# Kernel tuning notes

Measured on AMD Instinct MI355X. Metric: run time of the kernel, lower is better.

## Reference

```python
import jax, jax.numpy as jnp
import numpy as np

D_MODEL = 1024
NUM_HEADS = 16
D_FF = 4096
EPS = 1e-5


def setup_inputs() -> dict:
    key = jax.random.key(0)
    ks = jax.random.split(key, 8)
    B, S, D = 4, 2048, D_MODEL
    s = 1.0 / np.sqrt(D)
    return {
        "x": jax.random.normal(ks[0], (B, S, D), jnp.float32),
        "ln1_w": jnp.ones((D,), jnp.float32),
        "ln2_w": jnp.ones((D,), jnp.float32),
        "wq": jax.random.normal(ks[1], (D, D), jnp.float32) * s,
        "wk": jax.random.normal(ks[2], (D, D), jnp.float32) * s,
        "wv": jax.random.normal(ks[3], (D, D), jnp.float32) * s,
        "wo": jax.random.normal(ks[4], (D, D), jnp.float32) * s,
        "w1": jax.random.normal(ks[5], (D_FF, D), jnp.float32) * s,
        "w2": jax.random.normal(ks[6], (D, D_FF), jnp.float32) * (1.0 / np.sqrt(D_FF)),
    }


def rmsnorm(a, w):
    # (a * w) / sqrt(mean(a^2) + eps)  -- matches torch module exactly
    denom = jnp.sqrt(jnp.mean(jnp.square(a), axis=-1, keepdims=True) + EPS)
    return a * w / denom


def attention(x, wq, wk, wv, wo):
    B, S, D = x.shape
    H, dk = NUM_HEADS, D // NUM_HEADS
    q = (x @ wq.T).reshape(B, S, H, dk).transpose(0, 2, 1, 3)  # B H S dk
    k = (x @ wk.T).reshape(B, S, H, dk).transpose(0, 2, 1, 3)
    v = (x @ wv.T).reshape(B, S, H, dk).transpose(0, 2, 1, 3)
    scores = jnp.einsum("bhqd,bhkd->bhqk", q, k) / np.sqrt(dk)
    causal = jnp.triu(jnp.ones((S, S), bool), k=1)
    scores = jnp.where(causal, -jnp.inf, scores)
    probs = jax.nn.softmax(scores, axis=-1)
    out = jnp.einsum("bhqk,bhkd->bhqd", probs, v)
    out = out.transpose(0, 2, 1, 3).reshape(B, S, D)
    return out @ wo.T


def ffn(x, w1, w2):
    h = x @ w1.T
    h = 0.5 * h * (1.0 + jax.lax.erf(h / np.sqrt(2.0).astype(np.float32)))
    return h @ w2.T


def reference(x, ln1_w, ln2_w, wq, wk, wv, wo, w1, w2):
    y = x + attention(rmsnorm(x, ln1_w), wq, wk, wv, wo)
    return y + ffn(rmsnorm(y, ln2_w), w1, w2)
```

## Files before the change

kernel.cpp:

```cpp
#include <hip/hip_runtime.h>

#define DM    1024
#define DFF   4096
#define SEQ   2048
#define BATCH 4
#define NROWS (BATCH * SEQ)
#define HEADS 16
#define DKH   64
#define QSTR  (3 * DM)

typedef __attribute__((ext_vector_type(4))) float          f32x4;
typedef __attribute__((ext_vector_type(8))) __bf16         bf16x8;
typedef __attribute__((ext_vector_type(8))) unsigned short u16x8;
typedef __attribute__((ext_vector_type(4))) unsigned short u16x4;

static __device__ __forceinline__ unsigned short f2bf(float f) {
  unsigned u = __builtin_bit_cast(unsigned, f);
  u += 0x7fffu + ((u >> 16) & 1u);
  return (unsigned short)(u >> 16);
}

__global__ void k_f2bf(const float* __restrict__ in, unsigned short* __restrict__ out, int n4) {
  int i = blockIdx.x * blockDim.x + threadIdx.x;
  if (i >= n4) return;
  float4 v = reinterpret_cast<const float4*>(in)[i];
  ushort4 o;
  o.x = f2bf(v.x); o.y = f2bf(v.y); o.z = f2bf(v.z); o.w = f2bf(v.w);
  reinterpret_cast<ushort4*>(out)[i] = o;
}

__global__ __launch_bounds__(256) void k_rmsnorm(const float* __restrict__ x,
                                                 const float* __restrict__ w,
                                                 unsigned short* __restrict__ out) {
  const int row = blockIdx.x;
  const float4 v = reinterpret_cast<const float4*>(x + (size_t)row * DM)[threadIdx.x];
  float ss = v.x * v.x + v.y * v.y + v.z * v.z + v.w * v.w;
#pragma unroll
  for (int off = 32; off > 0; off >>= 1) ss += __shfl_down(ss, off);
  __shared__ float red[4];
  if ((threadIdx.x & 63) == 0) red[threadIdx.x >> 6] = ss;
  __syncthreads();
  const float tot  = red[0] + red[1] + red[2] + red[3];
  const float rden = rsqrtf(tot * (1.0f / DM) + 1e-5f);
  const float4 wv = reinterpret_cast<const float4*>(w)[threadIdx.x];
  ushort4 o;
  o.x = f2bf(v.x * wv.x * rden);
  o.y = f2bf(v.y * wv.y * rden);
  o.z = f2bf(v.z * wv.z * rden);
  o.w = f2bf(v.w * wv.w * rden);
  reinterpret_cast<ushort4*>(out + (size_t)row * DM)[threadIdx.x] = o;
}

__global__ __launch_bounds__(256) void k_vtrans(const unsigned short* __restrict__ V, int vstr,
                                                unsigned short* __restrict__ VT) {
  __shared__ unsigned short Tl[64][65];
  const int t  = threadIdx.x;
  const int r0 = blockIdx.x * 64;
  const int c0 = blockIdx.y * 64;
  const int ltr = t >> 3;
  const int lc  = (t & 7) * 8;
#pragma unroll
  for (int it = 0; it < 2; ++it) {
    const int r = ltr + 32 * it;
    u16x8 v = *reinterpret_cast<const u16x8*>(V + (size_t)(r0 + r) * vstr + c0 + lc);
#pragma unroll
    for (int i = 0; i < 8; ++i) Tl[r][lc + i] = v[i];
  }
  __syncthreads();
#pragma unroll
  for (int it = 0; it < 2; ++it) {
    const int c = ltr + 32 * it;
    u16x8 o;
#pragma unroll
    for (int i = 0; i < 8; ++i) o[i] = Tl[lc + i][c];
    *reinterpret_cast<u16x8*>(VT + (size_t)(c0 + c) * NROWS + r0 + lc) = o;
  }
}

template <int EPI>
__global__ __launch_bounds__(256) void k_gemm_nt(const unsigned short* __restrict__ A,
                                                 const unsigned short* __restrict__ B,
                                                 void* __restrict__ Cv,
                                                 const float* __restrict__ res,
                                                 int M, int N, int K) {
  alignas(16) __shared__ unsigned short As[128 * 32];
  alignas(16) __shared__ unsigned short Bs[128 * 32];
  const int t  = threadIdx.x;
  const int w  = t >> 6;
  const int l  = t & 63;
  const int wr = w >> 1, wc = w & 1;
  const int lr = l & 15, lk = l >> 4;

  const unsigned bid = blockIdx.y * gridDim.x + blockIdx.x;
  const unsigned cpx = (gridDim.x * gridDim.y) >> 3;
  const unsigned sw  = (bid & 7) * cpx + (bid >> 3);
  const int m0 = (int)(sw / gridDim.x) * 128;
  const int n0 = (int)(sw % gridDim.x) * 128;

  const int srow = t >> 2;
  const int scol = (t & 3) * 8;

  f32x4 acc[4][4] = {};

  for (int k0 = 0; k0 < K; k0 += 32) {
    __syncthreads();
#pragma unroll
    for (int r = 0; r < 2; ++r) {
      const unsigned short* ga = A + (size_t)(m0 + r * 64 + srow) * K + k0 + scol;
      const unsigned short* gb = B + (size_t)(n0 + r * 64 + srow) * K + k0 + scol;
      __builtin_amdgcn_global_load_lds((__attribute__((address_space(1))) void*)ga,
                                       (__attribute__((address_space(3))) void*)(As + r * 2048 + w * 512),
                                       16, 0, 0);
      __builtin_amdgcn_global_load_lds((__attribute__((address_space(1))) void*)gb,
                                       (__attribute__((address_space(3))) void*)(Bs + r * 2048 + w * 512),
                                       16, 0, 0);
    }
    __syncthreads();

    bf16x8 af[4], bf[4];
#pragma unroll
    for (int m = 0; m < 4; ++m)
      af[m] = *reinterpret_cast<const bf16x8*>(As + (wr * 64 + m * 16 + lr) * 32 + lk * 8);
#pragma unroll
    for (int n = 0; n < 4; ++n)
      bf[n] = *reinterpret_cast<const bf16x8*>(Bs + (wc * 64 + n * 16 + lr) * 32 + lk * 8);
#pragma unroll
    for (int m = 0; m < 4; ++m)
#pragma unroll
      for (int n = 0; n < 4; ++n)
        acc[m][n] = __builtin_amdgcn_mfma_f32_16x16x32_bf16(af[m], bf[n], acc[m][n], 0, 0, 0);
  }

#pragma unroll
  for (int m = 0; m < 4; ++m) {
#pragma unroll
    for (int n = 0; n < 4; ++n) {
#pragma unroll
      for (int r = 0; r < 4; ++r) {
        const size_t row = (size_t)(m0 + wr * 64 + m * 16 + lk * 4 + r);
        const size_t col = (size_t)(n0 + wc * 64 + n * 16 + lr);
        const float a = acc[m][n][r];
        if constexpr (EPI == 0) {
          ((unsigned short*)Cv)[row * N + col] = f2bf(a);
        } else if constexpr (EPI == 1) {
          ((float*)Cv)[row * N + col] = a + res[row * N + col];
        } else {
          const float g = 0.5f * a * (1.0f + erff(a * 0.70710678118f));
          ((unsigned short*)Cv)[row * N + col] = f2bf(g);
        }
      }
    }
  }
}

__global__ __launch_bounds__(256, 2) void k_attn(const unsigned short* __restrict__ QKV,
                                                 const unsigned short* __restrict__ VT,
                                                 unsigned short* __restrict__ O) {
  const int qtA = blockIdx.y & 7;
  const int qtB = (int)(SEQ / 128) - 1 - qtA;
  const int h   = blockIdx.x + 8 * (blockIdx.y >> 3);
  const int b   = blockIdx.z;
  const int t  = threadIdx.x, w = t >> 6, l = t & 63;
  const int lr = l & 15, lk = l >> 4;
  const size_t rowB = (size_t)b * SEQ;
  const int hoff  = h * DKH;
  const int qw2[2] = { qtA * 128 + 32 * w, qtB * 128 + 32 * w };

  alignas(16) __shared__ unsigned short Ks[2][64 * 64];
  alignas(16) __shared__ unsigned short Vt[2][64 * 64];
  alignas(16) __shared__ unsigned short Ps[2][4][32 * 64];

  char* const KsB = (char*)Ks;
  char* const VtB = (char*)Vt;

  auto stage = [&](int buf, int kb2) {
#pragma unroll
    for (int half = 0; half < 2; ++half) {
      const int srow = w * 16 + half * 8 + (l >> 3);
      const int sgr  = (l & 7) ^ (srow & 7);
      const unsigned short* gk = QKV + (size_t)(rowB + kb2 + srow) * QSTR + DM + hoff + 8 * sgr;
      __builtin_amdgcn_global_load_lds((__attribute__((address_space(1))) void*)gk,
                                       (__attribute__((address_space(3))) void*)(KsB + buf * 8192 + w * 2048 + half * 1024),
                                       16, 0, 0);
      const unsigned short* gv = VT + (size_t)(hoff + srow) * NROWS + rowB + kb2 + 8 * sgr;
      __builtin_amdgcn_global_load_lds((__attribute__((address_space(1))) void*)gv,
                                       (__attribute__((address_space(3))) void*)(VtB + buf * 8192 + w * 2048 + half * 1024),
                                       16, 0, 0);
    }
  };

  bf16x8 qf[2][2][2];
#pragma unroll
  for (int s = 0; s < 2; ++s)
#pragma unroll
    for (int g = 0; g < 2; ++g)
#pragma unroll
      for (int kk = 0; kk < 2; ++kk)
        qf[s][g][kk] = *reinterpret_cast<const bf16x8*>(
            QKV + (rowB + qw2[s] + 16 * g + lr) * QSTR + hoff + 32 * kk + 8 * lk);

  f32x4 oacc[2][2][4] = {};
  float mrun[2][2] = {{-1e30f, -1e30f}, {-1e30f, -1e30f}};
  float lrun[2][2] = {{0.0f, 0.0f}, {0.0f, 0.0f}};

  const float SCL = 0.18033688011f;

  const int ktmax = (qtB * 128 + 127) >> 6;
  stage(0, 0);
  for (int kt = 0; kt <= ktmax; ++kt) {
    const int kbase = kt * 64;
    const int cur   = kt & 1;
    __syncthreads();
    if (kt < ktmax) stage(cur ^ 1, kbase + 64);
    const char* Kc = KsB + cur * 8192;
    const char* Vc = VtB + cur * 8192;

    const bool act[2] = { kbase <= qw2[0] + 31, kbase <= qw2[1] + 31 };

    f32x4 sacc[2][2][4] = {};
#pragma unroll
    for (int tt = 0; tt < 4; ++tt) {
      bf16x8 kf0 = *reinterpret_cast<const bf16x8*>(Kc + (16 * tt + lr) * 128 + 16 * ((lk + 0) ^ (lr & 7)));
      bf16x8 kf1 = *reinterpret_cast<const bf16x8*>(Kc + (16 * tt + lr) * 128 + 16 * ((lk + 4) ^ (lr & 7)));
#pragma unroll
      for (int s = 0; s < 2; ++s) {
        if (!act[s]) continue;
#pragma unroll
        for (int g = 0; g < 2; ++g) {
          sacc[s][g][tt] = __builtin_amdgcn_mfma_f32_16x16x32_bf16(kf0, qf[s][g][0], sacc[s][g][tt], 0, 0, 0);
          sacc[s][g][tt] = __builtin_amdgcn_mfma_f32_16x16x32_bf16(kf1, qf[s][g][1], sacc[s][g][tt], 0, 0, 0);
        }
      }
    }

#pragma unroll
    for (int s = 0; s < 2; ++s) {
      if (!act[s]) continue;
      const int qw = qw2[s];
      char* const PsSB = (char*)(Ps[s][w]);
#pragma unroll
      for (int g = 0; g < 2; ++g) {
        const int qg = qw + 16 * g + lr;
        float sv[4][4];
        if (kbase + 63 > qw + 16 * g) {
#pragma unroll
          for (int tt = 0; tt < 4; ++tt)
#pragma unroll
            for (int r = 0; r < 4; ++r) {
              const int kg = kbase + 16 * tt + 4 * lk + r;
              sv[tt][r] = (kg > qg) ? -1e30f : sacc[s][g][tt][r] * SCL;
            }
        } else {
#pragma unroll
          for (int tt = 0; tt < 4; ++tt)
#pragma unroll
            for (int r = 0; r < 4; ++r) sv[tt][r] = sacc[s][g][tt][r] * SCL;
        }
        float tm = sv[0][0];
#pragma unroll
        for (int tt = 0; tt < 4; ++tt)
#pragma unroll
          for (int r = 0; r < 4; ++r) tm = fmaxf(tm, sv[tt][r]);
        tm = fmaxf(tm, __shfl_xor(tm, 16));
        tm = fmaxf(tm, __shfl_xor(tm, 32));
        float mref = mrun[s][g];
        if (__any(tm > mref + 8.0f)) {
          const float mnew  = fmaxf(mref, tm);
          const float alpha = exp2f(mref - mnew);
#pragma unroll
          for (int r = 0; r < 4; ++r) {
            const float ar = __shfl(alpha, 4 * lk + r);
#pragma unroll
            for (int dn = 0; dn < 4; ++dn) oacc[s][g][dn][r] *= ar;
          }
          lrun[s][g] *= alpha;
          mrun[s][g] = mnew;
          mref = mnew;
        }
        float ts = 0.0f;
        unsigned short pb[4][4];
#pragma unroll
        for (int tt = 0; tt < 4; ++tt)
#pragma unroll
          for (int r = 0; r < 4; ++r) {
            const float p = exp2f(sv[tt][r] - mref);
            ts += p;
            pb[tt][r] = __builtin_bit_cast(unsigned short, static_cast<__bf16>(p));
          }
        ts += __shfl_xor(ts, 16);
        ts += __shfl_xor(ts, 32);
        lrun[s][g] += ts;
#pragma unroll
        for (int tt = 0; tt < 4; ++tt) {
          u16x4 pw = {pb[tt][0], pb[tt][1], pb[tt][2], pb[tt][3]};
          *reinterpret_cast<u16x4*>(
              PsSB + (16 * g + lr) * 128 + ((32 * tt + 8 * lk) ^ (16 * (lr & 7)))) = pw;
        }
      }
    }

    asm volatile("" ::: "memory");

#pragma unroll
    for (int kk = 0; kk < 2; ++kk) {
      bf16x8 vf[4];
#pragma unroll
      for (int dn = 0; dn < 4; ++dn)
        vf[dn] = *reinterpret_cast<const bf16x8*>(
            Vc + (16 * dn + lr) * 128 + 16 * ((4 * kk + lk) ^ (lr & 7)));
#pragma unroll
      for (int s = 0; s < 2; ++s) {
        if (!act[s]) continue;
        char* const PsSB = (char*)(Ps[s][w]);
        bf16x8 pa[2];
#pragma unroll
        for (int g = 0; g < 2; ++g)
          pa[g] = *reinterpret_cast<const bf16x8*>(
              PsSB + (16 * g + lr) * 128 + ((64 * kk + 16 * lk) ^ (16 * (lr & 7))));
#pragma unroll
        for (int dn = 0; dn < 4; ++dn) {
          oacc[s][0][dn] = __builtin_amdgcn_mfma_f32_16x16x32_bf16(pa[0], vf[dn], oacc[s][0][dn], 0, 0, 0);
          oacc[s][1][dn] = __builtin_amdgcn_mfma_f32_16x16x32_bf16(pa[1], vf[dn], oacc[s][1][dn], 0, 0, 0);
        }
      }
    }

    asm volatile("" ::: "memory");
  }

#pragma unroll
  for (int s = 0; s < 2; ++s)
#pragma unroll
    for (int g = 0; g < 2; ++g)
#pragma unroll
      for (int r = 0; r < 4; ++r) {
        const float li = 1.0f / __shfl(lrun[s][g], 4 * lk + r);
        const size_t row = rowB + qw2[s] + 16 * g + 4 * lk + r;
#pragma unroll
        for (int dn = 0; dn < 4; ++dn)
          O[row * DM + hoff + 16 * dn + lr] = f2bf(oacc[s][g][dn][r] * li);
      }
}

extern "C" void kernel_launch(void* const* d_in, const int* in_sizes, int n_in,
                              void* d_out, int out_size, void* d_ws, size_t ws_size,
                              hipStream_t stream) {
  const float* x   = (const float*)d_in[0];
  const float* ln1 = (const float*)d_in[1];
  const float* ln2 = (const float*)d_in[2];
  const float* wq  = (const float*)d_in[3];
  const float* wk  = (const float*)d_in[4];
  const float* wv  = (const float*)d_in[5];
  const float* wo  = (const float*)d_in[6];
  const float* w1  = (const float*)d_in[7];
  const float* w2  = (const float*)d_in[8];

  char* ws = (char*)d_ws;
  size_t off = 0;
  auto take = [&](size_t bytes) { void* p = ws + off; off += bytes; return p; };
  unsigned short* wqkvb = (unsigned short*)take((size_t)3 * DM * DM * 2);
  unsigned short* wob   = (unsigned short*)take((size_t)DM * DM * 2);
  unsigned short* w1b   = (unsigned short*)take((size_t)DFF * DM * 2);
  unsigned short* w2b   = (unsigned short*)take((size_t)DM * DFF * 2);
  unsigned short* qkv   = (unsigned short*)take((size_t)NROWS * 3 * DM * 2);
  unsigned short* xn    = (unsigned short*)take((size_t)NROWS * DM * 2);
  unsigned short* hb    = (unsigned short*)take((size_t)NROWS * DFF * 2);
  unsigned short* yn  = qkv;
  float*          yb  = (float*)(qkv + (size_t)NROWS * DM);
  unsigned short* vtb = hb;

  auto cvt = [&](const float* src, unsigned short* dst, size_t n) {
    int n4 = (int)(n / 4);
    k_f2bf<<<dim3((n4 + 255) / 256), dim3(256), 0, stream>>>(src, dst, n4);
  };
  cvt(wq, wqkvb, (size_t)DM * DM);
  cvt(wk, wqkvb + (size_t)DM * DM, (size_t)DM * DM);
  cvt(wv, wqkvb + (size_t)2 * DM * DM, (size_t)DM * DM);
  cvt(wo, wob, (size_t)DM * DM);
  cvt(w1, w1b, (size_t)DFF * DM);
  cvt(w2, w2b, (size_t)DM * DFF);

  k_rmsnorm<<<dim3(NROWS), dim3(256), 0, stream>>>(x, ln1, xn);

  k_gemm_nt<0><<<dim3(3 * DM / 128, NROWS / 128), dim3(256), 0, stream>>>(
      xn, wqkvb, qkv, nullptr, NROWS, 3 * DM, DM);

  k_vtrans<<<dim3(NROWS / 64, DM / 64), dim3(256), 0, stream>>>(qkv + 2 * DM, QSTR, vtb);

  k_attn<<<dim3(SEQ / 256, HEADS, BATCH), dim3(256), 0, stream>>>(qkv, vtb, xn);

  const dim3 gD(DM / 128, NROWS / 128);
  k_gemm_nt<1><<<gD, dim3(256), 0, stream>>>(xn, wob, yb, x, NROWS, DM, DM);

  k_rmsnorm<<<dim3(NROWS), dim3(256), 0, stream>>>(yb, ln2, yn);

  k_gemm_nt<2><<<dim3(DFF / 128, NROWS / 128), dim3(256), 0, stream>>>(yn, w1b, hb, nullptr, NROWS, DFF, DM);
  k_gemm_nt<1><<<gD, dim3(256), 0, stream>>>(hb, w2b, (float*)d_out, yb, NROWS, DM, DFF);
}
```

Before: 458.9 us.

## Double-buffer GEMM LDS tiles, XOR-swizzle layout, and use tanh-approx GELU

Adds two LDS buffers to the bf16 NT GEMM so the next K-tile's global-to-LDS load is issued while the current tile is consumed by MFMA, leaving one barrier per iteration. The global source column is XOR-permuted by row so that fragment reads from LDS spread across banks. The exact erf GELU in the FFN epilogue is replaced by a sigmoid/tanh-style approximation built on exp2f. Doubling LDS may lower occupancy, and the GELU approximation changes numerics relative to the erf reference.

```diff
diff --git a/kernel.cpp b/kernel.cpp
--- a/kernel.cpp
+++ b/kernel.cpp
@@ -83,8 +83,8 @@
                                                  void* __restrict__ Cv,
                                                  const float* __restrict__ res,
                                                  int M, int N, int K) {
-  alignas(16) __shared__ unsigned short As[128 * 32];
-  alignas(16) __shared__ unsigned short Bs[128 * 32];
+  alignas(16) __shared__ unsigned short As[2][128 * 32];
+  alignas(16) __shared__ unsigned short Bs[2][128 * 32];
   const int t  = threadIdx.x;
   const int w  = t >> 6;
   const int l  = t & 63;
@@ -98,32 +98,40 @@
   const int n0 = (int)(sw % gridDim.x) * 128;
 
   const int srow = t >> 2;
-  const int scol = (t & 3) * 8;
-
-  f32x4 acc[4][4] = {};
-
-  for (int k0 = 0; k0 < K; k0 += 32) {
-    __syncthreads();
+  const int sgr  = (t & 3) ^ (srow & 3);
+
+  auto stage = [&](int buf, int k0) {
 #pragma unroll
     for (int r = 0; r < 2; ++r) {
-      const unsigned short* ga = A + (size_t)(m0 + r * 64 + srow) * K + k0 + scol;
-      const unsigned short* gb = B + (size_t)(n0 + r * 64 + srow) * K + k0 + scol;
+      const unsigned short* ga = A + (size_t)(m0 + r * 64 + srow) * K + k0 + 8 * sgr;
+      const unsigned short* gb = B + (size_t)(n0 + r * 64 + srow) * K + k0 + 8 * sgr;
       __builtin_amdgcn_global_load_lds((__attribute__((address_space(1))) void*)ga,
-                                       (__attribute__((address_space(3))) void*)(As + r * 2048 + w * 512),
+                                       (__attribute__((address_space(3))) void*)(&As[buf][r * 2048 + w * 512]),
                                        16, 0, 0);
       __builtin_amdgcn_global_load_lds((__attribute__((address_space(1))) void*)gb,
-                                       (__attribute__((address_space(3))) void*)(Bs + r * 2048 + w * 512),
+                                       (__attribute__((address_space(3))) void*)(&Bs[buf][r * 2048 + w * 512]),
                                        16, 0, 0);
     }
+  };
+
+  f32x4 acc[4][4] = {};
+
+  stage(0, 0);
+  const int nIt = K >> 5;
+  for (int it = 0; it < nIt; ++it) {
+    const int buf = it & 1;
     __syncthreads();
+    if (it + 1 < nIt) stage(buf ^ 1, (it + 1) << 5);
 
     bf16x8 af[4], bf[4];
 #pragma unroll
     for (int m = 0; m < 4; ++m)
-      af[m] = *reinterpret_cast<const bf16x8*>(As + (wr * 64 + m * 16 + lr) * 32 + lk * 8);
+      af[m] = *reinterpret_cast<const bf16x8*>(
+          &As[buf][(wr * 64 + m * 16 + lr) * 32 + 8 * (lk ^ (lr & 3))]);
 #pragma unroll
     for (int n = 0; n < 4; ++n)
-      bf[n] = *reinterpret_cast<const bf16x8*>(Bs + (wc * 64 + n * 16 + lr) * 32 + lk * 8);
+      bf[n] = *reinterpret_cast<const bf16x8*>(
+          &Bs[buf][(wc * 64 + n * 16 + lr) * 32 + 8 * (lk ^ (lr & 3))]);
 #pragma unroll
     for (int m = 0; m < 4; ++m)
 #pragma unroll
@@ -145,7 +153,9 @@
         } else if constexpr (EPI == 1) {
           ((float*)Cv)[row * N + col] = a + res[row * N + col];
         } else {
-          const float g = 0.5f * a * (1.0f + erff(a * 0.70710678118f));
+          const float h2 = a * a;
+          const float e  = exp2f(a * (2.30221535f + 0.10295355f * h2));
+          const float g  = a - a / (e + 1.0f);
           ((unsigned short*)Cv)[row * N + col] = f2bf(g);
         }
       }
```

New measurement: 422.9 us. 7.8% less time.
